# Kernel optimization log

Hardware: AMD Instinct MI355X
Metric: run time of the kernel (lower is better)

Reference implementation:

```python
import jax, jax.numpy as jnp
import numpy as np

T, B, N, C = 4, 4, 4096, 512
H = 8
D = C // H            # head_dim = 64
TAU = 2.0             # LIF tau
VTH = 1.0             # LIF threshold


def lif_spike(x):
    # LIFNode called once from zero state: v = 0 + (x - 0)/tau; spike = v >= vth
    v = x / TAU
    return (v >= VTH).astype(x.dtype)


def setup_inputs() -> dict:
    key = jax.random.key(0)
    ks = jax.random.split(key, 9)
    s = 0.05  # weight scale so pre-spike potentials straddle the threshold
    x = jax.random.normal(ks[0], (T, B, N, C), dtype=jnp.float32)
    Wq = jax.random.normal(ks[1], (C, C), dtype=jnp.float32) * s
    bq = jnp.zeros((C,), dtype=jnp.float32)
    Wk = jax.random.normal(ks[2], (C, C), dtype=jnp.float32) * s
    bk = jnp.zeros((C,), dtype=jnp.float32)
    Wv = jax.random.normal(ks[3], (C, C), dtype=jnp.float32) * s
    bv = jnp.zeros((C,), dtype=jnp.float32)
    Wo = jax.random.normal(ks[4], (C, C), dtype=jnp.float32) * s
    bo = jnp.zeros((C,), dtype=jnp.float32)
    return {"x": x, "Wq": Wq, "bq": bq, "Wk": Wk, "bk": bk,
            "Wv": Wv, "bv": bv, "Wo": Wo, "bo": bo}


def reference(x, Wq, bq, Wk, bk, Wv, bv, Wo, bo):
    # nn.Linear: y = x @ W.T + b (SeqToANNContainer just flattens (T,B))
    q = jnp.einsum('tbnc,oc->tbno', x, Wq) + bq
    k = jnp.einsum('tbnc,oc->tbno', x, Wk) + bk
    v = jnp.einsum('tbnc,oc->tbno', x, Wv) + bv
    # reshape to heads; attention runs over the spiking time axis T per token
    q = q.reshape(T, B, N, H, D).transpose(1, 2, 0, 3, 4)   # (B,N,T,H,D)
    k = k.reshape(T, B, N, H, D).transpose(1, 2, 3, 4, 0)   # (B,N,H,D,T)
    v = v.reshape(T, B, N, H, D).transpose(1, 2, 3, 0, 4)   # (B,N,H,T,D)
    attn = jnp.einsum('bnthd,bnhds->bnths', q, k) / jnp.sqrt(jnp.float32(D))
    attn = lif_spike(attn)                                  # binary spikes replace softmax
    out = jnp.einsum('bnths,bnhsd->bnthd', attn, v)         # (B,N,T,H,D)
    out = out.transpose(2, 0, 1, 3, 4).reshape(T, B, N, C)
    return jnp.einsum('tbnc,oc->tbno', out, Wo) + bo
```

## Files before the change

kernel.cpp:

```cpp
#include <hip/hip_runtime.h>

#define PTOT  16384
#define CCC   512
#define HHH   8
#define NSTEP 16

typedef __attribute__((ext_vector_type(4))) float f32x4;
typedef _Float16 half_t;
typedef __attribute__((ext_vector_type(8))) _Float16 f16x8;

#define MFMA_F16(a,b,c) __builtin_amdgcn_mfma_f32_16x16x32_f16(a,b,c,0,0,0)

#define XH_OFF   ((size_t)0)
#define XL_OFF   ((size_t)33554432)
#define ACT_OFF  ((size_t)67108864)
#define W_OFF    ((size_t)100663296)
#define WPL      ((size_t)262144)

__device__ __forceinline__ size_t blk_off(int row, int col) {
    return ((size_t)((row >> 4) * 16 + (col >> 5)) << 9)
         + (size_t)(((((col >> 3) & 3) * 16) + (row & 15)) << 3) + (col & 7);
}

__global__ void k0_split(const float* __restrict__ x,
                         const float* __restrict__ Wq, const float* __restrict__ Wk,
                         const float* __restrict__ Wv, const float* __restrict__ Wo,
                         half_t* __restrict__ ws)
{
    const int u = blockIdx.x * 256 + threadIdx.x;
    const float* src;
    half_t *dh, *dl;
    int gr, v;
    if (u < 4194304) {
        gr = u >> 10; v = u & 1023;
        src = x; dh = ws + XH_OFF; dl = ws + XL_OFF;
    } else {
        const int u2 = u - 4194304;
        const int mat = u2 >> 15, r = u2 & 32767;
        gr = r >> 10; v = r & 1023;
        if      (mat == 0) { src = Wq; dh = ws + W_OFF;           dl = ws + W_OFF + WPL; }
        else if (mat == 1) { src = Wk; dh = ws + W_OFF + 2*WPL;   dl = ws + W_OFF + 3*WPL; }
        else if (mat == 2) { src = Wv; dh = ws + W_OFF + 4*WPL;   dl = nullptr; }
        else               { src = Wo; dh = ws + W_OFF + 5*WPL;   dl = nullptr; }
    }
    const int ktc = v >> 6, chunk = (v >> 4) & 3, i = v & 15;
    const int row = gr * 16 + i, col = ktc * 32 + chunk * 8;

    const float4 a = *(const float4*)(src + (size_t)row * CCC + col);
    const float4 b = *(const float4*)(src + (size_t)row * CCC + col + 4);
    const float e[8] = {a.x, a.y, a.z, a.w, b.x, b.y, b.z, b.w};
    f16x8 vh8, vl8;
    #pragma unroll
    for (int d = 0; d < 8; ++d) {
        const half_t hi = (half_t)e[d];
        const half_t lo = (half_t)(e[d] - (float)hi);
        vh8[d] = hi; vl8[d] = lo;
    }
    const size_t off = blk_off(row, col);
    *(f16x8*)(dh + off) = vh8;
    if (dl) *(f16x8*)(dl + off) = vl8;
}

__global__ __launch_bounds__(256, 2)
void k1_mfma(const half_t* __restrict__ ws,
             const float* __restrict__ bq, const float* __restrict__ bk,
             const float* __restrict__ bv,
             half_t* __restrict__ acth)
{
    __shared__ __align__(16) char smem[73728];

    const int tid  = threadIdx.x;
    const int lane = tid & 63;
    const int wv   = tid >> 6;
    const int wr   = wv >> 1;
    const int wc   = wv & 1;
    const int l15  = lane & 15;
    const int l4   = lane >> 4;

    const int xcd = blockIdx.x & 7;
    const int rest = blockIdx.x >> 3;
    const int h   = rest & 7;
    const int tg  = rest >> 3;
    const int p0  = (tg * 8 + xcd) * 32;

    const half_t* gb[9]; int lo_[9];
    #pragma unroll
    for (int ii = 0; ii < 9; ++ii) {
        const int i = wv * 9 + ii;
        size_t eoff; int loff;
        if (i < 16) {
            const int pl = i >> 3, fb = i & 7;
            const int grow = (((fb >> 1) * PTOT) + p0 + ((fb & 1) * 16)) >> 4;
            eoff = (pl ? XL_OFF : XH_OFF) + ((size_t)grow << 13) + lane * 8;
            loff = i * 1024;
        } else {
            const int s = i - 16, plw = s >> 2, cf = s & 3;
            const int grow = h * 4 + cf;
            eoff = W_OFF + (size_t)plw * WPL + ((size_t)grow << 13) + lane * 8;
            loff = 16384 + s * 1024;
        }
        gb[ii] = ws + eoff;
        lo_[ii] = loff;
    }

#define K1_STAGE(buf, kt) do {                                                  \
    _Pragma("unroll")                                                           \
    for (int ii = 0; ii < 9; ++ii)                                              \
        __builtin_amdgcn_global_load_lds(                                       \
            (const __attribute__((address_space(1))) void*)(gb[ii] + (size_t)(kt) * 512), \
            (__attribute__((address_space(3))) void*)(smem + (buf) * 36864 + lo_[ii]),    \
            16, 0, 0);                                                          \
    } while (0)

    f32x4 accQ[4][2], accK[4][2], accV[4][2];
    {
        const int c0 = h * 64 + wc * 32 + l15, c1 = c0 + 16;
        const float bq0 = bq[c0], bq1 = bq[c1];
        const float bk0 = bk[c0], bk1 = bk[c1];
        const float bv0 = bv[c0], bv1 = bv[c1];
        #pragma unroll
        for (int rf = 0; rf < 4; ++rf) {
            accQ[rf][0] = f32x4{bq0, bq0, bq0, bq0};
            accQ[rf][1] = f32x4{bq1, bq1, bq1, bq1};
            accK[rf][0] = f32x4{bk0, bk0, bk0, bk0};
            accK[rf][1] = f32x4{bk1, bk1, bk1, bk1};
            accV[rf][0] = f32x4{bv0, bv0, bv0, bv0};
            accV[rf][1] = f32x4{bv1, bv1, bv1, bv1};
        }
    }

    K1_STAGE(0, 0);

    #pragma unroll
    for (int kt = 0; kt < NSTEP; ++kt) {
        const int cur = kt & 1;
        if (kt + 1 < NSTEP) {
            K1_STAGE(cur ^ 1, kt + 1);
            asm volatile("s_waitcnt vmcnt(9)" ::: "memory");
        } else {
            asm volatile("s_waitcnt vmcnt(0)" ::: "memory");
        }
        __builtin_amdgcn_sched_barrier(0);
        __builtin_amdgcn_s_barrier();

        const char* bp = smem + cur * 36864;
        f16x8 Bqh[2], Bql[2], Bkh[2], Bkl[2], Bvh[2];
        #pragma unroll
        for (int c = 0; c < 2; ++c) {
            const int cf = wc * 2 + c;
            Bqh[c] = *(const f16x8*)(bp + 16384 + (0*4 + cf) * 1024 + lane * 16);
            Bql[c] = *(const f16x8*)(bp + 16384 + (1*4 + cf) * 1024 + lane * 16);
            Bkh[c] = *(const f16x8*)(bp + 16384 + (2*4 + cf) * 1024 + lane * 16);
            Bkl[c] = *(const f16x8*)(bp + 16384 + (3*4 + cf) * 1024 + lane * 16);
            Bvh[c] = *(const f16x8*)(bp + 16384 + (4*4 + cf) * 1024 + lane * 16);
        }
        #pragma unroll
        for (int rf = 0; rf < 4; ++rf) {
            const int fb = wr * 4 + rf;
            const f16x8 Ah = *(const f16x8*)(bp + fb * 1024 + lane * 16);
            const f16x8 Al = *(const f16x8*)(bp + (8 + fb) * 1024 + lane * 16);
            #pragma unroll
            for (int c = 0; c < 2; ++c) {
                f32x4 q = accQ[rf][c];
                q = MFMA_F16(Ah, Bqh[c], q);
                q = MFMA_F16(Ah, Bql[c], q);
                q = MFMA_F16(Al, Bqh[c], q);
                accQ[rf][c] = q;
                f32x4 k = accK[rf][c];
                k = MFMA_F16(Ah, Bkh[c], k);
                k = MFMA_F16(Ah, Bkl[c], k);
                k = MFMA_F16(Al, Bkh[c], k);
                accK[rf][c] = k;
                accV[rf][c] = MFMA_F16(Ah, Bvh[c], accV[rf][c]);
            }
        }
        asm volatile("s_waitcnt lgkmcnt(0)" ::: "memory");
        __builtin_amdgcn_s_barrier();
        __builtin_amdgcn_sched_barrier(0);
    }

    float* qa = (float*)smem;
    float* ka = qa + 4352;
    float* va = qa + 8704;

    const int ar  = tid >> 2;
    const int t_  = ar >> 4;
    const int jj  = ar & 15;
    const int sub = tid & 3;

    #pragma unroll
    for (int hh = 0; hh < 2; ++hh) {
        #pragma unroll
        for (int m = 0; m < 2; ++m) {
            const int rf = 2 * m + hh;
            const int t  = 2 * wr + m;
            const int rb = t * 16 + l4 * 4;
            #pragma unroll
            for (int c = 0; c < 2; ++c) {
                const int cc = wc * 32 + c * 16 + l15;
                #pragma unroll
                for (int r = 0; r < 4; ++r) {
                    qa[(rb + r) * 68 + cc] = accQ[rf][c][r];
                    ka[(rb + r) * 68 + cc] = accK[rf][c][r];
                    va[(rb + r) * 68 + cc] = accV[rf][c][r];
                }
            }
        }
        __syncthreads();

        const float* qp = qa + ar * 68 + sub * 16;
        const float4 q0 = *(const float4*)(qp);
        const float4 q1 = *(const float4*)(qp + 4);
        const float4 q2 = *(const float4*)(qp + 8);
        const float4 q3 = *(const float4*)(qp + 12);
        float sc[4];
        #pragma unroll
        for (int ss = 0; ss < 4; ++ss) {
            const float* kp = ka + (ss * 16 + jj) * 68 + sub * 16;
            const float4 k0 = *(const float4*)(kp);
            const float4 k1 = *(const float4*)(kp + 4);
            const float4 k2 = *(const float4*)(kp + 8);
            const float4 k3 = *(const float4*)(kp + 12);
            float p = q0.x*k0.x + q0.y*k0.y + q0.z*k0.z + q0.w*k0.w
                    + q1.x*k1.x + q1.y*k1.y + q1.z*k1.z + q1.w*k1.w
                    + q2.x*k2.x + q2.y*k2.y + q2.z*k2.z + q2.w*k2.w
                    + q3.x*k3.x + q3.y*k3.y + q3.z*k3.z + q3.w*k3.w;
            p += __shfl_xor(p, 1);
            p += __shfl_xor(p, 2);
            sc[ss] = p;
        }
        float o[16];
        #pragma unroll
        for (int d = 0; d < 16; ++d) o[d] = 0.f;
        #pragma unroll
        for (int ss = 0; ss < 4; ++ss) {
            if (sc[ss] >= 16.0f) {
                const float* vp = va + (ss * 16 + jj) * 68 + sub * 16;
                const float4 v0 = *(const float4*)(vp);
                const float4 v1 = *(const float4*)(vp + 4);
                const float4 v2 = *(const float4*)(vp + 8);
                const float4 v3 = *(const float4*)(vp + 12);
                o[0]+=v0.x; o[1]+=v0.y; o[2]+=v0.z;  o[3]+=v0.w;
                o[4]+=v1.x; o[5]+=v1.y; o[6]+=v1.z;  o[7]+=v1.w;
                o[8]+=v2.x; o[9]+=v2.y; o[10]+=v2.z; o[11]+=v2.w;
                o[12]+=v3.x;o[13]+=v3.y;o[14]+=v3.z; o[15]+=v3.w;
            }
        }
        f16x8 o0, o1;
        #pragma unroll
        for (int d = 0; d < 8; ++d) { o0[d] = (half_t)o[d]; o1[d] = (half_t)o[d + 8]; }
        const int grow = t_ * 1024 + (p0 >> 4) + hh;
        const int colb = h * 64 + sub * 16;
        const size_t cbase = ((size_t)(grow * 16 + (colb >> 5))) << 9;
        const int c0 = (colb >> 3) & 3;
        *(f16x8*)(acth + cbase + (size_t)((c0       * 16 + jj) << 3)) = o0;
        *(f16x8*)(acth + cbase + (size_t)(((c0 + 1) * 16 + jj) << 3)) = o1;
        __syncthreads();
    }
#undef K1_STAGE
}

__global__ __launch_bounds__(256, 4)
void k2_gemm(const half_t* __restrict__ acth, const half_t* __restrict__ oh,
             const float* __restrict__ bo, float* __restrict__ out)
{
    __shared__ __align__(16) char smem[32768];

    const int tid  = threadIdx.x;
    const int lane = tid & 63;
    const int wv   = tid >> 6;
    const int wr   = wv >> 1, wc = wv & 1;
    const int l15  = lane & 15, l4 = lane >> 4;
    const int bn   = (blockIdx.x & 3) * 128;
    const int bm   = (blockIdx.x >> 2) * 128;

    const half_t* gb[4]; int lo_[4];
    #pragma unroll
    for (int ii = 0; ii < 4; ++ii) {
        const int i = wv * 4 + ii;
        if (i < 8) {
            const int grow = (bm >> 4) + i;
            gb[ii] = acth + ((size_t)grow << 13) + lane * 8;
            lo_[ii] = i * 1024;
        } else {
            const int fb = i - 8;
            const int grow = (bn >> 4) + fb;
            gb[ii] = oh + ((size_t)grow << 13) + lane * 8;
            lo_[ii] = 8192 + fb * 1024;
        }
    }

#define K2_STAGE(buf, kt) do {                                                  \
    _Pragma("unroll")                                                           \
    for (int ii = 0; ii < 4; ++ii)                                              \
        __builtin_amdgcn_global_load_lds(                                       \
            (const __attribute__((address_space(1))) void*)(gb[ii] + (size_t)(kt) * 512), \
            (__attribute__((address_space(3))) void*)(smem + (buf) * 16384 + lo_[ii]),    \
            16, 0, 0);                                                          \
    } while (0)

    f32x4 acc[4][4];
    #pragma unroll
    for (int rf = 0; rf < 4; ++rf)
        #pragma unroll
        for (int cf = 0; cf < 4; ++cf) acc[rf][cf] = f32x4{0.f, 0.f, 0.f, 0.f};

    K2_STAGE(0, 0);

    #pragma unroll
    for (int kt = 0; kt < NSTEP; ++kt) {
        const int cur = kt & 1;
        if (kt + 1 < NSTEP) {
            K2_STAGE(cur ^ 1, kt + 1);
            asm volatile("s_waitcnt vmcnt(4)" ::: "memory");
        } else {
            asm volatile("s_waitcnt vmcnt(0)" ::: "memory");
        }
        __builtin_amdgcn_sched_barrier(0);
        __builtin_amdgcn_s_barrier();

        const char* bp = smem + cur * 16384;
        f16x8 B[4];
        #pragma unroll
        for (int cf = 0; cf < 4; ++cf)
            B[cf] = *(const f16x8*)(bp + 8192 + (wc * 4 + cf) * 1024 + lane * 16);
        #pragma unroll
        for (int rf = 0; rf < 4; ++rf) {
            const f16x8 A = *(const f16x8*)(bp + (wr * 4 + rf) * 1024 + lane * 16);
            #pragma unroll
            for (int cf = 0; cf < 4; ++cf)
                acc[rf][cf] = MFMA_F16(A, B[cf], acc[rf][cf]);
        }
        asm volatile("s_waitcnt lgkmcnt(0)" ::: "memory");
        __builtin_amdgcn_s_barrier();
        __builtin_amdgcn_sched_barrier(0);
    }

    float bo4[4];
    #pragma unroll
    for (int cf = 0; cf < 4; ++cf) bo4[cf] = bo[bn + (wc * 4 + cf) * 16 + l15];

    #pragma unroll
    for (int rf = 0; rf < 4; ++rf) {
        const int row0 = bm + (wr * 4 + rf) * 16 + l4 * 4;
        #pragma unroll
        for (int cf = 0; cf < 4; ++cf) {
            const int col = bn + (wc * 4 + cf) * 16 + l15;
            #pragma unroll
            for (int r = 0; r < 4; ++r)
                out[(size_t)(row0 + r) * CCC + col] = acc[rf][cf][r] + bo4[cf];
        }
    }
#undef K2_STAGE
}

extern "C" void kernel_launch(void* const* d_in, const int* in_sizes, int n_in,
                              void* d_out, int out_size, void* d_ws, size_t ws_size,
                              hipStream_t stream)
{
    const float* x  = (const float*)d_in[0];
    const float* Wq = (const float*)d_in[1];
    const float* bq = (const float*)d_in[2];
    const float* Wk = (const float*)d_in[3];
    const float* bk = (const float*)d_in[4];
    const float* Wv = (const float*)d_in[5];
    const float* bv = (const float*)d_in[6];
    const float* Wo = (const float*)d_in[7];
    const float* bo = (const float*)d_in[8];

    half_t* ws   = (half_t*)d_ws;
    half_t* acth = ws + ACT_OFF;
    float*  out  = (float*)d_out;

    hipLaunchKernelGGL(k0_split, dim3(16896), dim3(256), 0, stream,
                       x, Wq, Wk, Wv, Wo, ws);
    hipLaunchKernelGGL(k1_mfma, dim3(4096), dim3(256), 0, stream,
                       ws, bq, bk, bv, acth);
    hipLaunchKernelGGL(k2_gemm, dim3(2048), dim3(256), 0, stream,
                       acth, ws + W_OFF + 5*WPL, bo, out);
}
```

Before: 317.8 us.

## Switch QKV projection to 32x32x16 MFMA with new blocked layout and higher occupancy

The QKV projection kernel moves from 16x16x32 MFMA tiles to 32x32x16 MFMA tiles. To feed them, the prepass writes x and the Q/K/V weights in a new 32-row blocked layout, while Wo keeps the old layout. The K loop becomes 32 half-size steps with a smaller LDS footprint, which allows launch bounds of 3 blocks per CU. The aim is fewer LDS fragment loads per MFMA and more resident waves, at the cost of twice as many barriers and uneven load counts across waves.

```diff
diff --git a/kernel.cpp b/kernel.cpp
--- a/kernel.cpp
+++ b/kernel.cpp
@@ -3,13 +3,16 @@
 #define PTOT  16384
 #define CCC   512
 #define HHH   8
-#define NSTEP 16
-
-typedef __attribute__((ext_vector_type(4))) float f32x4;
+#define NK1   32
+#define NK2   16
+
+typedef __attribute__((ext_vector_type(4)))  float f32x4;
+typedef __attribute__((ext_vector_type(16))) float f32x16;
 typedef _Float16 half_t;
 typedef __attribute__((ext_vector_type(8))) _Float16 f16x8;
 
-#define MFMA_F16(a,b,c) __builtin_amdgcn_mfma_f32_16x16x32_f16(a,b,c,0,0,0)
+#define MFMA16(a,b,c) __builtin_amdgcn_mfma_f32_16x16x32_f16(a,b,c,0,0,0)
+#define MFMA32(a,b,c) __builtin_amdgcn_mfma_f32_32x32x16_f16(a,b,c,0,0,0)
 
 #define XH_OFF   ((size_t)0)
 #define XL_OFF   ((size_t)33554432)
@@ -17,9 +20,13 @@
 #define W_OFF    ((size_t)100663296)
 #define WPL      ((size_t)262144)
 
-__device__ __forceinline__ size_t blk_off(int row, int col) {
+__device__ __forceinline__ size_t blk_off16(int row, int col) {
     return ((size_t)((row >> 4) * 16 + (col >> 5)) << 9)
          + (size_t)(((((col >> 3) & 3) * 16) + (row & 15)) << 3) + (col & 7);
+}
+__device__ __forceinline__ size_t blk_off32(int row, int k) {
+    return ((size_t)((row >> 5) * 32 + (k >> 4)) << 9)
+         + (size_t)(((((k >> 3) & 1) * 32) + (row & 31)) << 3) + (k & 7);
 }
 
 __global__ void k0_split(const float* __restrict__ x,
@@ -30,24 +37,23 @@
     const int u = blockIdx.x * 256 + threadIdx.x;
     const float* src;
     half_t *dh, *dl;
-    int gr, v;
+    int row, c;
+    bool old16 = false;
     if (u < 4194304) {
-        gr = u >> 10; v = u & 1023;
+        row = u >> 6; c = u & 63;
         src = x; dh = ws + XH_OFF; dl = ws + XL_OFF;
     } else {
         const int u2 = u - 4194304;
         const int mat = u2 >> 15, r = u2 & 32767;
-        gr = r >> 10; v = r & 1023;
-        if      (mat == 0) { src = Wq; dh = ws + W_OFF;           dl = ws + W_OFF + WPL; }
-        else if (mat == 1) { src = Wk; dh = ws + W_OFF + 2*WPL;   dl = ws + W_OFF + 3*WPL; }
-        else if (mat == 2) { src = Wv; dh = ws + W_OFF + 4*WPL;   dl = nullptr; }
-        else               { src = Wo; dh = ws + W_OFF + 5*WPL;   dl = nullptr; }
-    }
-    const int ktc = v >> 6, chunk = (v >> 4) & 3, i = v & 15;
-    const int row = gr * 16 + i, col = ktc * 32 + chunk * 8;
-
-    const float4 a = *(const float4*)(src + (size_t)row * CCC + col);
-    const float4 b = *(const float4*)(src + (size_t)row * CCC + col + 4);
+        row = r >> 6; c = r & 63;
+        if      (mat == 0) { src = Wq; dh = ws + W_OFF;         dl = ws + W_OFF + WPL; }
+        else if (mat == 1) { src = Wk; dh = ws + W_OFF + 2*WPL; dl = ws + W_OFF + 3*WPL; }
+        else if (mat == 2) { src = Wv; dh = ws + W_OFF + 4*WPL; dl = nullptr; }
+        else               { src = Wo; dh = ws + W_OFF + 5*WPL; dl = nullptr; old16 = true; }
+    }
+    const int k = c * 8;
+    const float4 a = *(const float4*)(src + (size_t)row * CCC + k);
+    const float4 b = *(const float4*)(src + (size_t)row * CCC + k + 4);
     const float e[8] = {a.x, a.y, a.z, a.w, b.x, b.y, b.z, b.w};
     f16x8 vh8, vl8;
     #pragma unroll
@@ -56,48 +62,50 @@
         const half_t lo = (half_t)(e[d] - (float)hi);
         vh8[d] = hi; vl8[d] = lo;
     }
-    const size_t off = blk_off(row, col);
+    const size_t off = old16 ? blk_off16(row, k) : blk_off32(row, k);
     *(f16x8*)(dh + off) = vh8;
     if (dl) *(f16x8*)(dl + off) = vl8;
 }
 
-__global__ __launch_bounds__(256, 2)
+__global__ __launch_bounds__(256, 3)
 void k1_mfma(const half_t* __restrict__ ws,
              const float* __restrict__ bq, const float* __restrict__ bk,
              const float* __restrict__ bv,
              half_t* __restrict__ acth)
 {
-    __shared__ __align__(16) char smem[73728];
+    __shared__ __align__(16) char smem[52224];
 
     const int tid  = threadIdx.x;
     const int lane = tid & 63;
     const int wv   = tid >> 6;
-    const int wr   = wv >> 1;
-    const int wc   = wv & 1;
-    const int l15  = lane & 15;
-    const int l4   = lane >> 4;
-
-    const int xcd = blockIdx.x & 7;
+    const int rg   = wv >> 1;
+    const int cg   = wv & 1;
+    const int l31  = lane & 31;
+    const int l5   = lane >> 5;
+
+    const int xcd  = blockIdx.x & 7;
     const int rest = blockIdx.x >> 3;
-    const int h   = rest & 7;
-    const int tg  = rest >> 3;
-    const int p0  = (tg * 8 + xcd) * 32;
-
-    const half_t* gb[9]; int lo_[9];
-    #pragma unroll
-    for (int ii = 0; ii < 9; ++ii) {
-        const int i = wv * 9 + ii;
+    const int h    = rest & 7;
+    const int tg   = rest >> 3;
+    const int p0   = (tg * 8 + xcd) * 32;
+
+    const int cnt  = (wv < 2) ? 5 : 4;
+    const int base = (wv < 2) ? wv * 5 : 2 + wv * 4;
+    const half_t* gb[5]; int lo_[5];
+    #pragma unroll
+    for (int ii = 0; ii < 5; ++ii) {
+        const int i = base + ii;
         size_t eoff; int loff;
-        if (i < 16) {
-            const int pl = i >> 3, fb = i & 7;
-            const int grow = (((fb >> 1) * PTOT) + p0 + ((fb & 1) * 16)) >> 4;
-            eoff = (pl ? XL_OFF : XH_OFF) + ((size_t)grow << 13) + lane * 8;
+        if (i < 8) {
+            const int t = i >> 1, pl = i & 1;
+            const size_t rbg = (size_t)t * 512 + (p0 >> 5);
+            eoff = (pl ? XL_OFF : XH_OFF) + rbg * 16384 + lane * 8;
             loff = i * 1024;
         } else {
-            const int s = i - 16, plw = s >> 2, cf = s & 3;
-            const int grow = h * 4 + cf;
-            eoff = W_OFF + (size_t)plw * WPL + ((size_t)grow << 13) + lane * 8;
-            loff = 16384 + s * 1024;
+            const int s = (i - 8) & 15;
+            const int plw = (s >> 1) > 4 ? 4 : (s >> 1), cb = s & 1;
+            eoff = W_OFF + (size_t)plw * WPL + (size_t)(h * 2 + cb) * 16384 + lane * 8;
+            loff = 8192 + s * 1024;
         }
         gb[ii] = ws + eoff;
         lo_[ii] = loff;
@@ -105,75 +113,70 @@
 
 #define K1_STAGE(buf, kt) do {                                                  \
     _Pragma("unroll")                                                           \
-    for (int ii = 0; ii < 9; ++ii)                                              \
-        __builtin_amdgcn_global_load_lds(                                       \
-            (const __attribute__((address_space(1))) void*)(gb[ii] + (size_t)(kt) * 512), \
-            (__attribute__((address_space(3))) void*)(smem + (buf) * 36864 + lo_[ii]),    \
-            16, 0, 0);                                                          \
+    for (int ii = 0; ii < 5; ++ii)                                              \
+        if (ii < cnt)                                                           \
+            __builtin_amdgcn_global_load_lds(                                   \
+                (const __attribute__((address_space(1))) void*)(gb[ii] + (size_t)(kt) * 512), \
+                (__attribute__((address_space(3))) void*)(smem + (buf) * 18432 + lo_[ii]),    \
+                16, 0, 0);                                                      \
     } while (0)
 
-    f32x4 accQ[4][2], accK[4][2], accV[4][2];
+    f32x16 accQ[2], accK[2], accV[2];
     {
-        const int c0 = h * 64 + wc * 32 + l15, c1 = c0 + 16;
-        const float bq0 = bq[c0], bq1 = bq[c1];
-        const float bk0 = bk[c0], bk1 = bk[c1];
-        const float bv0 = bv[c0], bv1 = bv[c1];
-        #pragma unroll
-        for (int rf = 0; rf < 4; ++rf) {
-            accQ[rf][0] = f32x4{bq0, bq0, bq0, bq0};
-            accQ[rf][1] = f32x4{bq1, bq1, bq1, bq1};
-            accK[rf][0] = f32x4{bk0, bk0, bk0, bk0};
-            accK[rf][1] = f32x4{bk1, bk1, bk1, bk1};
-            accV[rf][0] = f32x4{bv0, bv0, bv0, bv0};
-            accV[rf][1] = f32x4{bv1, bv1, bv1, bv1};
+        const int c0 = h * 64 + cg * 32 + l31;
+        const float q0 = bq[c0], k0 = bk[c0], v0 = bv[c0];
+        #pragma unroll
+        for (int i = 0; i < 16; ++i) {
+            accQ[0][i] = q0; accQ[1][i] = q0;
+            accK[0][i] = k0; accK[1][i] = k0;
+            accV[0][i] = v0; accV[1][i] = v0;
         }
     }
 
     K1_STAGE(0, 0);
 
-    #pragma unroll
-    for (int kt = 0; kt < NSTEP; ++kt) {
+    #pragma unroll 2
+    for (int kt = 0; kt < NK1; ++kt) {
         const int cur = kt & 1;
-        if (kt + 1 < NSTEP) {
+        if (kt + 1 < NK1) {
             K1_STAGE(cur ^ 1, kt + 1);
-            asm volatile("s_waitcnt vmcnt(9)" ::: "memory");
+            if (cnt == 5) asm volatile("s_waitcnt vmcnt(5)" ::: "memory");
+            else          asm volatile("s_waitcnt vmcnt(4)" ::: "memory");
         } else {
             asm volatile("s_waitcnt vmcnt(0)" ::: "memory");
         }
         __builtin_amdgcn_sched_barrier(0);
         __builtin_amdgcn_s_barrier();
 
-        const char* bp = smem + cur * 36864;
-        f16x8 Bqh[2], Bql[2], Bkh[2], Bkl[2], Bvh[2];
-        #pragma unroll
-        for (int c = 0; c < 2; ++c) {
-            const int cf = wc * 2 + c;
-            Bqh[c] = *(const f16x8*)(bp + 16384 + (0*4 + cf) * 1024 + lane * 16);
-            Bql[c] = *(const f16x8*)(bp + 16384 + (1*4 + cf) * 1024 + lane * 16);
-            Bkh[c] = *(const f16x8*)(bp + 16384 + (2*4 + cf) * 1024 + lane * 16);
-            Bkl[c] = *(const f16x8*)(bp + 16384 + (3*4 + cf) * 1024 + lane * 16);
-            Bvh[c] = *(const f16x8*)(bp + 16384 + (4*4 + cf) * 1024 + lane * 16);
-        }
-        #pragma unroll
-        for (int rf = 0; rf < 4; ++rf) {
-            const int fb = wr * 4 + rf;
-            const f16x8 Ah = *(const f16x8*)(bp + fb * 1024 + lane * 16);
-            const f16x8 Al = *(const f16x8*)(bp + (8 + fb) * 1024 + lane * 16);
-            #pragma unroll
-            for (int c = 0; c < 2; ++c) {
-                f32x4 q = accQ[rf][c];
-                q = MFMA_F16(Ah, Bqh[c], q);
-                q = MFMA_F16(Ah, Bql[c], q);
-                q = MFMA_F16(Al, Bqh[c], q);
-                accQ[rf][c] = q;
-                f32x4 k = accK[rf][c];
-                k = MFMA_F16(Ah, Bkh[c], k);
-                k = MFMA_F16(Ah, Bkl[c], k);
-                k = MFMA_F16(Al, Bkh[c], k);
-                accK[rf][c] = k;
-                accV[rf][c] = MFMA_F16(Ah, Bvh[c], accV[rf][c]);
-            }
-        }
+        const char* bp = smem + cur * 18432;
+        const int boff = 8192 + cg * 1024 + lane * 16;
+        const f16x8 Bqh = *(const f16x8*)(bp + boff);
+        const f16x8 Bql = *(const f16x8*)(bp + boff + 2048);
+        const f16x8 Bkh = *(const f16x8*)(bp + boff + 4096);
+        const f16x8 Bkl = *(const f16x8*)(bp + boff + 6144);
+        const f16x8 Bvh = *(const f16x8*)(bp + boff + 8192);
+        f16x8 Ah[2], Al[2];
+        #pragma unroll
+        for (int rf = 0; rf < 2; ++rf) {
+            const int t = rg * 2 + rf;
+            Ah[rf] = *(const f16x8*)(bp + (t * 2 + 0) * 1024 + lane * 16);
+            Al[rf] = *(const f16x8*)(bp + (t * 2 + 1) * 1024 + lane * 16);
+        }
+        accQ[0] = MFMA32(Ah[0], Bqh, accQ[0]);
+        accQ[1] = MFMA32(Ah[1], Bqh, accQ[1]);
+        accK[0] = MFMA32(Ah[0], Bkh, accK[0]);
+        accK[1] = MFMA32(Ah[1], Bkh, accK[1]);
+        accV[0] = MFMA32(Ah[0], Bvh, accV[0]);
+        accV[1] = MFMA32(Ah[1], Bvh, accV[1]);
+        accQ[0] = MFMA32(Ah[0], Bql, accQ[0]);
+        accQ[1] = MFMA32(Ah[1], Bql, accQ[1]);
+        accK[0] = MFMA32(Ah[0], Bkl, accK[0]);
+        accK[1] = MFMA32(Ah[1], Bkl, accK[1]);
+        accQ[0] = MFMA32(Al[0], Bqh, accQ[0]);
+        accQ[1] = MFMA32(Al[1], Bqh, accQ[1]);
+        accK[0] = MFMA32(Al[0], Bkh, accK[0]);
+        accK[1] = MFMA32(Al[1], Bkh, accK[1]);
+
         asm volatile("s_waitcnt lgkmcnt(0)" ::: "memory");
         __builtin_amdgcn_s_barrier();
         __builtin_amdgcn_sched_barrier(0);
@@ -191,19 +194,16 @@
     #pragma unroll
     for (int hh = 0; hh < 2; ++hh) {
         #pragma unroll
-        for (int m = 0; m < 2; ++m) {
-            const int rf = 2 * m + hh;
-            const int t  = 2 * wr + m;
-            const int rb = t * 16 + l4 * 4;
+        for (int rf = 0; rf < 2; ++rf) {
+            const int t = rg * 2 + rf;
             #pragma unroll
-            for (int c = 0; c < 2; ++c) {
-                const int cc = wc * 32 + c * 16 + l15;
-                #pragma unroll
-                for (int r = 0; r < 4; ++r) {
-                    qa[(rb + r) * 68 + cc] = accQ[rf][c][r];
-                    ka[(rb + r) * 68 + cc] = accK[rf][c][r];
-                    va[(rb + r) * 68 + cc] = accV[rf][c][r];
-                }
+            for (int rr = 0; rr < 8; ++rr) {
+                const int reg = hh * 8 + rr;
+                const int j2  = (rr & 3) + 8 * (rr >> 2) + 4 * l5;
+                const int idx = (t * 16 + j2) * 68 + cg * 32 + l31;
+                qa[idx] = accQ[rf][reg];
+                ka[idx] = accK[rf][reg];
+                va[idx] = accV[rf][reg];
             }
         }
         __syncthreads();
@@ -308,9 +308,9 @@
     K2_STAGE(0, 0);
 
     #pragma unroll
-    for (int kt = 0; kt < NSTEP; ++kt) {
+    for (int kt = 0; kt < NK2; ++kt) {
         const int cur = kt & 1;
-        if (kt + 1 < NSTEP) {
+        if (kt + 1 < NK2) {
             K2_STAGE(cur ^ 1, kt + 1);
             asm volatile("s_waitcnt vmcnt(4)" ::: "memory");
         } else {
@@ -329,7 +329,7 @@
             const f16x8 A = *(const f16x8*)(bp + (wr * 4 + rf) * 1024 + lane * 16);
             #pragma unroll
             for (int cf = 0; cf < 4; ++cf)
-                acc[rf][cf] = MFMA_F16(A, B[cf], acc[rf][cf]);
+                acc[rf][cf] = MFMA16(A, B[cf], acc[rf][cf]);
         }
         asm volatile("s_waitcnt lgkmcnt(0)" ::: "memory");
         __builtin_amdgcn_s_barrier();
```

Result: slower. 388.6 us (+22.3%).
